# Kernel optimization log

Measured on AMD Instinct MI355X. Metric: run time of the kernel, lower is better.

## Reference

```python
import jax, jax.numpy as jnp
import numpy as np

N, E = 50000, 400000
FN, FE, FG = 32, 16, 16
H1, H2 = 256, 128


def seg_mean(x, idx, n):
    # mean of edge rows per segment; empty segments -> 0 (scatter_mean semantics)
    s = jax.ops.segment_sum(x, idx, num_segments=n)
    c = jax.ops.segment_sum(jnp.ones((x.shape[0], 1), x.dtype), idx, num_segments=n)
    return s / jnp.maximum(c, 1.0)


def setup_inputs() -> dict:
    key = jax.random.key(0)
    ks = jax.random.split(key, 32)
    g = lambda k, shape, s=0.05: jax.random.normal(k, shape, dtype=jnp.float32) * s
    return {
        'nodes': g(ks[0], (N, FN), 1.0),
        'edges': g(ks[1], (E, FE), 1.0),
        'globals_u': g(ks[2], (FG,), 1.0),
        'senders': jax.random.randint(ks[3], (E,), 0, N, dtype=jnp.int32),
        'receivers': jax.random.randint(ks[4], (E,), 0, N, dtype=jnp.int32),
        'We1': g(ks[5], (FE, H1)), 'be1': jnp.zeros((H1,), jnp.float32),
        'Wn1': g(ks[6], (FN, H1)), 'Win1': g(ks[7], (H1, H1)), 'Wout1': g(ks[8], (H1, H1)), 'bn1': jnp.zeros((H1,), jnp.float32),
        'Wu1': g(ks[9], (FG, H1)), 'Wgn1': g(ks[10], (H1, H1)), 'Wge1': g(ks[11], (H1, H1)), 'bu1': jnp.zeros((H1,), jnp.float32),
        'We2': g(ks[12], (H1, H2)), 'be2': jnp.zeros((H2,), jnp.float32),
        'Wn2': g(ks[13], (H1, H2)), 'Win2': g(ks[14], (H2, H2)), 'Wout2': g(ks[15], (H2, H2)), 'bn2': jnp.zeros((H2,), jnp.float32),
        'Wu2': g(ks[16], (H1, H2)), 'Wgn2': g(ks[17], (H2, H2)), 'Wge2': g(ks[18], (H2, H2)), 'bu2': jnp.zeros((H2,), jnp.float32),
    }


def reference(nodes, edges, globals_u, senders, receivers,
              We1, be1, Wn1, Win1, Wout1, bn1, Wu1, Wgn1, Wge1, bu1,
              We2, be2, Wn2, Win2, Wout2, bn2, Wu2, Wgn2, Wge2, bu2):
    n = nodes.shape[0]
    # --- block 1 (width 256) ---
    e1 = jax.nn.relu(edges @ We1 + be1)                                  # [E, H1]
    inc1 = seg_mean(e1, receivers, n)                                    # avg incoming edges per node
    out1 = seg_mean(e1, senders, n)                                      # avg outgoing edges per node
    n1 = jax.nn.relu(nodes @ Wn1 + inc1 @ Win1 + out1 @ Wout1 + bn1)     # [N, H1]
    u1 = jax.nn.relu(globals_u @ Wu1 + n1.mean(0) @ Wgn1 + e1.mean(0) @ Wge1 + bu1)  # [H1]
    # --- block 2 (width 128) ---
    e2 = jax.nn.relu(e1 @ We2 + be2)                                     # [E, H2]
    inc2 = seg_mean(e2, receivers, n)
    out2 = seg_mean(e2, senders, n)
    n2 = jax.nn.relu(n1 @ Wn2 + inc2 @ Win2 + out2 @ Wout2 + bn2)        # [N, H2]
    u2 = jax.nn.relu(u1 @ Wu2 + n2.mean(0) @ Wgn2 + e2.mean(0) @ Wge2 + bu2)  # [H2]
    return n2, e2, u2
```

## Files before the change

kernel.cpp:

```cpp
#include <hip/hip_runtime.h>
#include <hip/hip_bf16.h>
#include <stdint.h>

#define NN 50000
#define NE 400000
#define FN 32
#define FE 16
#define FG 16
#define H1 256
#define H2 128
#define M2 (2*NN)
#define SCAN_B 391
#define NPART 256

typedef unsigned short u16;
typedef __bf16 bfv8 __attribute__((ext_vector_type(8)));
typedef float f32v4 __attribute__((ext_vector_type(4)));
typedef u16 usv2 __attribute__((ext_vector_type(2)));
typedef u16 usv4 __attribute__((ext_vector_type(4)));
typedef u16 usv8 __attribute__((ext_vector_type(8)));

#define APK 264
#define AP2 136
#define EP1 40


__device__ __forceinline__ u16 f2b(float x){
  __hip_bfloat16 h = __float2bfloat16(x);
  return *reinterpret_cast<u16*>(&h);
}
__device__ __forceinline__ float bf2f(u16 u){
  union{uint32_t i; float f;} v; v.i = ((uint32_t)u) << 16; return v.f;
}

template<int NCK, int NNT, int PITCH>
__device__ __forceinline__ void gemm_tiles(const u16* a_s, const u16* __restrict__ pB,
                                           int w, int l, f32v4* acc)
{
  const int lr = l & 15, q = l >> 4;
  const bfv8* bp = (const bfv8*)pB;
  for (int ck = 0; ck < NCK; ck++){
    bfv8 a = *(const bfv8*)&a_s[(w*16 + lr)*PITCH + ck*32 + q*8];
    #pragma unroll
    for (int nt = 0; nt < NNT; nt++){
      bfv8 b = bp[(ck*NNT + nt)*64 + l];
      acc[nt] = __builtin_amdgcn_mfma_f32_16x16x32_bf16(a, b, acc[nt], 0, 0, 0);
    }
  }
}

template<int C4PR_LOG2>
__device__ __forceinline__ void stage_rows(u16* a_s, const float* __restrict__ src,
                                           long n0, int t)
{
  const int c4pr = 1 << C4PR_LOG2;
  for (int idx = t; idx < 64*c4pr; idx += 256){
    int row = idx >> C4PR_LOG2, c4 = idx & (c4pr - 1);
    long n = n0 + row;
    float x0=0.f, x1=0.f, x2=0.f, x3=0.f;
    if (n < NN){
      const float4 v = *(const float4*)&src[(n << (C4PR_LOG2 + 2)) + c4*4];
      x0 = v.x; x1 = v.y; x2 = v.z; x3 = v.w;
    }
    usv4 o; o.x = f2b(x0); o.y = f2b(x1); o.z = f2b(x2); o.w = f2b(x3);
    *(usv4*)&a_s[row*APK + c4*4] = o;
  }
}

struct PD { const float* src; u16* dst; int K, N, Ks, perm; };
struct PackArgs { PD d[8]; };

__global__ __launch_bounds__(64) void pack_weights(PackArgs A){
  int b = blockIdx.x, l = threadIdx.x;
  int mi = 0, base = 0;
  for (; mi < 8; mi++){
    int tiles = (A.d[mi].K >> 5) * (A.d[mi].N >> 4);
    if (b < base + tiles) break;
    base += tiles;
  }
  const PD d = A.d[mi];
  const int tile = b - base;
  const int ntn = d.N >> 4;
  const int ck = tile / ntn, nt = tile % ntn;
  const int lr = l & 15, q = l >> 4;
  const int col = nt*16 + lr;
  usv8 o;
  #pragma unroll
  for (int j = 0; j < 8; j++){
    int k = ck*32 + q*8 + j;
    int sk = (d.perm == 1) ? (((k & 15) << 4) | (k >> 4))
           : (d.perm == 2) ? (((k & 7) << 4) | (k >> 3))
           : k;
    o[j] = (k < d.Ks) ? f2b(d.src[(long)sk * d.N + col]) : (u16)0;
  }
  *(usv8*)&d.dst[((long)tile*64 + l)*8] = o;
}

__global__ __launch_bounds__(256) void csr_count(const int* __restrict__ recv,
    const int* __restrict__ send, int* cnt, int* pos_in, int* pos_out)
{
  int e = blockIdx.x*256 + threadIdx.x;
  if (e >= NE) return;
  pos_in [e] = atomicAdd(&cnt[recv[e]], 1);
  pos_out[e] = atomicAdd(&cnt[NN + send[e]], 1);
}

__global__ __launch_bounds__(256) void scan_blocks(const int* __restrict__ cnt,
    int* off, int* btot)
{
  __shared__ int s[256];
  int b = blockIdx.x, t = threadIdx.x;
  int i = b*256 + t;
  int v = (i < M2) ? cnt[i] : 0;
  s[t] = v; __syncthreads();
  int acc = v;
  for (int d = 1; d < 256; d <<= 1){
    int add = (t >= d) ? s[t-d] : 0;
    __syncthreads();
    acc += add; s[t] = acc;
    __syncthreads();
  }
  if (i < M2) off[i] = acc - v;
  if (t == 255) btot[b] = acc;
}

__global__ __launch_bounds__(256) void scan_tops(int* btot){
  __shared__ int s[512], ts[256];
  int t = threadIdx.x;
  s[t]     = (t < SCAN_B) ? btot[t] : 0;
  s[256+t] = (256+t < SCAN_B) ? btot[256+t] : 0;
  __syncthreads();
  int a0 = s[2*t], a1 = s[2*t+1];
  int tot = a0 + a1;
  ts[t] = tot; __syncthreads();
  int acc = tot;
  for (int d = 1; d < 256; d <<= 1){
    int add = (t >= d) ? ts[t-d] : 0;
    __syncthreads();
    acc += add; ts[t] = acc;
    __syncthreads();
  }
  int excl = acc - tot;
  if (2*t   < SCAN_B) btot[2*t]   = excl;
  if (2*t+1 < SCAN_B) btot[2*t+1] = excl + a0;
}

__global__ __launch_bounds__(256) void scan_fix(int* off, const int* __restrict__ btot){
  int i = blockIdx.x*256 + threadIdx.x;
  if (i < M2) off[i] += btot[blockIdx.x];
}

__global__ __launch_bounds__(256) void csr_fill(const int* __restrict__ recv,
    const int* __restrict__ send, const int* __restrict__ off,
    const int* __restrict__ pos_in, const int* __restrict__ pos_out, int* lis)
{
  int e = blockIdx.x*256 + threadIdx.x;
  if (e >= NE) return;
  lis[off[recv[e]]      + pos_in [e]] = e;
  lis[off[NN + send[e]] + pos_out[e]] = e;
}

__global__ __launch_bounds__(256) void edge1_kernel(const float* __restrict__ edges,
    const u16* __restrict__ pWe1, const float* __restrict__ be1,
    u16* __restrict__ e1b, float* __restrict__ e1p)
{
  __shared__ __align__(16) u16 a_es[64*EP1];
  __shared__ float cs_s[H1];
  __shared__ float bs[H1];
  const int t = threadIdx.x;
  const long e0 = (long)blockIdx.x * 64;
  const int w = t >> 6, l = t & 63, lr = l & 15, q = l >> 4;
  cs_s[t] = 0.f;
  bs[t] = be1[t];
  {
    int row = t >> 2, c4 = t & 3;
    float4 v = *(const float4*)&edges[(e0 + row)*FE + c4*4];
    usv4 o = { f2b(v.x), f2b(v.y), f2b(v.z), f2b(v.w) };
    *(usv4*)&a_es[row*EP1 + c4*4] = o;
    *(usv4*)&a_es[row*EP1 + 16 + c4*4] = (usv4){0,0,0,0};
  }
  __syncthreads();
  f32v4 acc[16];
  #pragma unroll
  for (int nt = 0; nt < 16; nt++) acc[nt] = (f32v4){0.f,0.f,0.f,0.f};
  gemm_tiles<1,16,EP1>(a_es, pWe1, w, l, acc);

  #pragma unroll
  for (int nt = 0; nt < 16; nt++){
    const float b = bs[nt*16 + lr];
    float part = 0.f;
    #pragma unroll
    for (int r = 0; r < 4; r++){
      float v = fmaxf(acc[nt][r] + b, 0.f);
      acc[nt][r] = v; part += v;
    }
    part += __shfl_xor(part, 16);
    part += __shfl_xor(part, 32);
    if (q == 0) atomicAdd(&cs_s[nt*16 + lr], part);
  }
  usv8 ob0[4], ob1[4];
  #pragma unroll
  for (int r = 0; r < 4; r++){
    #pragma unroll
    for (int h = 0; h < 8; h++){ ob0[r][h] = f2b(acc[h][r]); ob1[r][h] = f2b(acc[8+h][r]); }
  }
  __syncthreads();
  atomicAdd(&e1p[(blockIdx.x & (NPART-1))*H1 + t], cs_s[t]);
  #pragma unroll
  for (int r = 0; r < 4; r++){
    const int m = w*16 + q*4 + r;
    *(usv8*)&e1b[(e0 + m)*H1 + lr*16]     = ob0[r];
    *(usv8*)&e1b[(e0 + m)*H1 + lr*16 + 8] = ob1[r];
  }
}

template<bool WRB>
__global__ __launch_bounds__(256) void e2_kernel(float* __restrict__ e2f,
    const u16* __restrict__ pWe2, const float* __restrict__ be2, float* __restrict__ e2p,
    u16* __restrict__ e2b)
{
  __shared__ __align__(16) u16 a_s[64*APK];
  __shared__ float cs_s[H2];
  __shared__ float bs[H2];
  const int t = threadIdx.x;
  const long e0 = (long)blockIdx.x * 64;
  const int w = t >> 6, l = t & 63, lr = l & 15, q = l >> 4;
  if (t < H2){ cs_s[t] = 0.f; bs[t] = be2[t]; }
  const u16* e1u = (const u16*)e2f;
  for (int idx = t; idx < 64*32; idx += 256){
    int row = idx >> 5, ch = idx & 31;
    usv8 v = *(const usv8*)&e1u[(e0 + row)*H1 + ch*8];
    *(usv8*)&a_s[row*APK + ch*8] = v;
  }
  __syncthreads();
  f32v4 acc[8];
  #pragma unroll
  for (int nt = 0; nt < 8; nt++) acc[nt] = (f32v4){0.f,0.f,0.f,0.f};
  gemm_tiles<8,8,APK>(a_s, pWe2, w, l, acc);

  #pragma unroll
  for (int nt = 0; nt < 8; nt++){
    const float b = bs[nt*16 + lr];
    float part = 0.f;
    #pragma unroll
    for (int r = 0; r < 4; r++){
      float v = fmaxf(acc[nt][r] + b, 0.f);
      acc[nt][r] = v; part += v;
    }
    part += __shfl_xor(part, 16);
    part += __shfl_xor(part, 32);
    if (q == 0) atomicAdd(&cs_s[nt*16 + lr], part);
  }
  __syncthreads();
  float* fl = (float*)a_s;
  #pragma unroll
  for (int r = 0; r < 4; r++){
    const int m = w*16 + q*4 + r;
    const int sw = (m & 7) * 4;
    #pragma unroll
    for (int nt = 0; nt < 8; nt++)
      fl[m*128 + ((nt*16 + lr) ^ sw)] = acc[nt][r];
  }
  __syncthreads();
  if (t < H2) atomicAdd(&e2p[(blockIdx.x & (NPART-1))*H2 + t], cs_s[t]);
  {
    const int row = t >> 2, c = t & 3;
    const int sw = (row & 7) * 4;
    #pragma unroll
    for (int k = 0; k < 8; k++){
      const int wi = (c*32 + k*4) ^ sw;
      float4 v = *(const float4*)&fl[row*128 + wi];
      *(float4*)&e2f[(e0 + row)*H2 + c*32 + k*4] = v;
    }
  }
  if (WRB){
    #pragma unroll
    for (int r = 0; r < 4; r++){
      const int m = w*16 + q*4 + r;
      usv8 ob;
      #pragma unroll
      for (int nt = 0; nt < 8; nt++) ob[nt] = f2b(acc[nt][r]);
      *(usv8*)&e2b[(e0 + m)*H2 + lr*8] = ob;
    }
  }
}

template<int PITCH>
__device__ __forceinline__ void gather_h1(u16* a_s, const u16* __restrict__ src,
    const int* roff, const int* __restrict__ lis, int w, int l)
{
  for (int rr = 0; rr < 16; rr++){
    int r = w + rr*4;
    int rs = roff[r], re = roff[r+1];
    float s0=0.f, s1=0.f, s2=0.f, s3=0.f;
    int j = rs;
    for (; j + 8 <= re; j += 8){
      int i0=lis[j],i1=lis[j+1],i2=lis[j+2],i3=lis[j+3];
      int i4=lis[j+4],i5=lis[j+5],i6=lis[j+6],i7=lis[j+7];
      usv4 a0 = *(const usv4*)&src[(long)i0*H1 + l*4];
      usv4 a1 = *(const usv4*)&src[(long)i1*H1 + l*4];
      usv4 a2 = *(const usv4*)&src[(long)i2*H1 + l*4];
      usv4 a3 = *(const usv4*)&src[(long)i3*H1 + l*4];
      usv4 a4 = *(const usv4*)&src[(long)i4*H1 + l*4];
      usv4 a5 = *(const usv4*)&src[(long)i5*H1 + l*4];
      usv4 a6 = *(const usv4*)&src[(long)i6*H1 + l*4];
      usv4 a7 = *(const usv4*)&src[(long)i7*H1 + l*4];
      s0 += ((bf2f(a0.x)+bf2f(a1.x)) + (bf2f(a2.x)+bf2f(a3.x)))
          + ((bf2f(a4.x)+bf2f(a5.x)) + (bf2f(a6.x)+bf2f(a7.x)));
      s1 += ((bf2f(a0.y)+bf2f(a1.y)) + (bf2f(a2.y)+bf2f(a3.y)))
          + ((bf2f(a4.y)+bf2f(a5.y)) + (bf2f(a6.y)+bf2f(a7.y)));
      s2 += ((bf2f(a0.z)+bf2f(a1.z)) + (bf2f(a2.z)+bf2f(a3.z)))
          + ((bf2f(a4.z)+bf2f(a5.z)) + (bf2f(a6.z)+bf2f(a7.z)));
      s3 += ((bf2f(a0.w)+bf2f(a1.w)) + (bf2f(a2.w)+bf2f(a3.w)))
          + ((bf2f(a4.w)+bf2f(a5.w)) + (bf2f(a6.w)+bf2f(a7.w)));
    }
    for (; j + 4 <= re; j += 4){
      int i0=lis[j],i1=lis[j+1],i2=lis[j+2],i3=lis[j+3];
      usv4 a0 = *(const usv4*)&src[(long)i0*H1 + l*4];
      usv4 a1 = *(const usv4*)&src[(long)i1*H1 + l*4];
      usv4 a2 = *(const usv4*)&src[(long)i2*H1 + l*4];
      usv4 a3 = *(const usv4*)&src[(long)i3*H1 + l*4];
      s0 += (bf2f(a0.x)+bf2f(a1.x)) + (bf2f(a2.x)+bf2f(a3.x));
      s1 += (bf2f(a0.y)+bf2f(a1.y)) + (bf2f(a2.y)+bf2f(a3.y));
      s2 += (bf2f(a0.z)+bf2f(a1.z)) + (bf2f(a2.z)+bf2f(a3.z));
      s3 += (bf2f(a0.w)+bf2f(a1.w)) + (bf2f(a2.w)+bf2f(a3.w));
    }
    for (; j < re; ++j){
      int i0 = lis[j];
      usv4 a0 = *(const usv4*)&src[(long)i0*H1 + l*4];
      s0 += bf2f(a0.x); s1 += bf2f(a0.y); s2 += bf2f(a0.z); s3 += bf2f(a0.w);
    }
    float rd = 1.f / fmaxf((float)(re - rs), 1.f);
    usv4 o = { f2b(s0*rd), f2b(s1*rd), f2b(s2*rd), f2b(s3*rd) };
    *(usv4*)&a_s[r*PITCH + l*4] = o;
  }
}

template<int PITCH>
__device__ __forceinline__ void gather_h2(u16* a_s, const float* __restrict__ src,
    const int* roff, const int* __restrict__ lis, int w, int l)
{
  for (int rr = 0; rr < 16; rr++){
    int r = w + rr*4;
    int rs = roff[r], re = roff[r+1];
    float s0=0.f, s1=0.f;
    int j = rs;
    for (; j + 8 <= re; j += 8){
      int i0=lis[j],i1=lis[j+1],i2=lis[j+2],i3=lis[j+3];
      int i4=lis[j+4],i5=lis[j+5],i6=lis[j+6],i7=lis[j+7];
      float2 a0 = *(const float2*)&src[(long)i0*H2 + l*2];
      float2 a1 = *(const float2*)&src[(long)i1*H2 + l*2];
      float2 a2 = *(const float2*)&src[(long)i2*H2 + l*2];
      float2 a3 = *(const float2*)&src[(long)i3*H2 + l*2];
      float2 a4 = *(const float2*)&src[(long)i4*H2 + l*2];
      float2 a5 = *(const float2*)&src[(long)i5*H2 + l*2];
      float2 a6 = *(const float2*)&src[(long)i6*H2 + l*2];
      float2 a7 = *(const float2*)&src[(long)i7*H2 + l*2];
      s0 += ((a0.x+a1.x) + (a2.x+a3.x)) + ((a4.x+a5.x) + (a6.x+a7.x));
      s1 += ((a0.y+a1.y) + (a2.y+a3.y)) + ((a4.y+a5.y) + (a6.y+a7.y));
    }
    for (; j + 4 <= re; j += 4){
      int i0=lis[j],i1=lis[j+1],i2=lis[j+2],i3=lis[j+3];
      float2 a0 = *(const float2*)&src[(long)i0*H2 + l*2];
      float2 a1 = *(const float2*)&src[(long)i1*H2 + l*2];
      float2 a2 = *(const float2*)&src[(long)i2*H2 + l*2];
      float2 a3 = *(const float2*)&src[(long)i3*H2 + l*2];
      s0 += (a0.x+a1.x) + (a2.x+a3.x);
      s1 += (a0.y+a1.y) + (a2.y+a3.y);
    }
    for (; j < re; ++j){
      int i0 = lis[j];
      float2 a0 = *(const float2*)&src[(long)i0*H2 + l*2];
      s0 += a0.x; s1 += a0.y;
    }
    float rd = 1.f / fmaxf((float)(re - rs), 1.f);
    usv2 o = { f2b(s0*rd), f2b(s1*rd) };
    *(usv2*)&a_s[r*PITCH + l*2] = o;
  }
}

template<int PITCH>
__device__ __forceinline__ void gather_h2b(u16* a_s, const u16* __restrict__ src,
    const int* roff, const int* __restrict__ lis, int w, int l)
{
  for (int rr = 0; rr < 16; rr++){
    int r = w + rr*4;
    int rs = roff[r], re = roff[r+1];
    float s0=0.f, s1=0.f;
    int j = rs;
    for (; j + 8 <= re; j += 8){
      int i0=lis[j],i1=lis[j+1],i2=lis[j+2],i3=lis[j+3];
      int i4=lis[j+4],i5=lis[j+5],i6=lis[j+6],i7=lis[j+7];
      usv2 a0 = *(const usv2*)&src[(long)i0*H2 + l*2];
      usv2 a1 = *(const usv2*)&src[(long)i1*H2 + l*2];
      usv2 a2 = *(const usv2*)&src[(long)i2*H2 + l*2];
      usv2 a3 = *(const usv2*)&src[(long)i3*H2 + l*2];
      usv2 a4 = *(const usv2*)&src[(long)i4*H2 + l*2];
      usv2 a5 = *(const usv2*)&src[(long)i5*H2 + l*2];
      usv2 a6 = *(const usv2*)&src[(long)i6*H2 + l*2];
      usv2 a7 = *(const usv2*)&src[(long)i7*H2 + l*2];
      s0 += ((bf2f(a0.x)+bf2f(a1.x)) + (bf2f(a2.x)+bf2f(a3.x)))
          + ((bf2f(a4.x)+bf2f(a5.x)) + (bf2f(a6.x)+bf2f(a7.x)));
      s1 += ((bf2f(a0.y)+bf2f(a1.y)) + (bf2f(a2.y)+bf2f(a3.y)))
          + ((bf2f(a4.y)+bf2f(a5.y)) + (bf2f(a6.y)+bf2f(a7.y)));
    }
    for (; j + 4 <= re; j += 4){
      int i0=lis[j],i1=lis[j+1],i2=lis[j+2],i3=lis[j+3];
      usv2 a0 = *(const usv2*)&src[(long)i0*H2 + l*2];
      usv2 a1 = *(const usv2*)&src[(long)i1*H2 + l*2];
      usv2 a2 = *(const usv2*)&src[(long)i2*H2 + l*2];
      usv2 a3 = *(const usv2*)&src[(long)i3*H2 + l*2];
      s0 += (bf2f(a0.x)+bf2f(a1.x)) + (bf2f(a2.x)+bf2f(a3.x));
      s1 += (bf2f(a0.y)+bf2f(a1.y)) + (bf2f(a2.y)+bf2f(a3.y));
    }
    for (; j < re; ++j){
      int i0 = lis[j];
      usv2 a0 = *(const usv2*)&src[(long)i0*H2 + l*2];
      s0 += bf2f(a0.x); s1 += bf2f(a0.y);
    }
    float rd = 1.f / fmaxf((float)(re - rs), 1.f);
    usv2 o = { f2b(s0*rd), f2b(s1*rd) };
    *(usv2*)&a_s[r*PITCH + l*2] = o;
  }
}

__global__ __launch_bounds__(256, 4) void node1_kernel(
    const float* __restrict__ nodes, const u16* __restrict__ e1b,
    const int* __restrict__ off, const int* __restrict__ lis,
    const u16* __restrict__ pWn1, const u16* __restrict__ pWin1, const u16* __restrict__ pWout1,
    const float* __restrict__ bn1, u16* __restrict__ n1b, float* __restrict__ n1p)
{
  __shared__ __align__(16) u16 a_s[64*APK];
  __shared__ int roff[65], roff2[65];
  __shared__ float cs_s[H1];
  __shared__ float bs[H1];
  const int t = threadIdx.x;
  const long n0 = (long)blockIdx.x * 64;
  const int w = t >> 6, l = t & 63, lr = l & 15, q = l >> 4;

  cs_s[t] = 0.f;
  bs[t] = bn1[t];
  if (t <= 64){
    long idx = n0 + t;
    roff [t] = (idx >= NN) ? NE     : off[idx];
    roff2[t] = (idx >= NN) ? 2*NE   : off[NN + idx];
  }
  __syncthreads();

  f32v4 acc[16];
  #pragma unroll
  for (int nt = 0; nt < 16; nt++) acc[nt] = (f32v4){0.f,0.f,0.f,0.f};

  gather_h1<APK>(a_s, e1b, roff, lis, w, l);
  __syncthreads();
  gemm_tiles<8,16,APK>(a_s, pWin1, w, l, acc);
  __syncthreads();

  gather_h1<APK>(a_s, e1b, roff2, lis, w, l);
  __syncthreads();
  gemm_tiles<8,16,APK>(a_s, pWout1, w, l, acc);
  __syncthreads();

  stage_rows<3>(a_s, nodes, n0, t);
  __syncthreads();
  gemm_tiles<1,16,APK>(a_s, pWn1, w, l, acc);

  #pragma unroll
  for (int nt = 0; nt < 16; nt++){
    const float b = bs[nt*16 + lr];
    float part = 0.f;
    #pragma unroll
    for (int r = 0; r < 4; r++){
      const long n = n0 + w*16 + q*4 + r;
      float v = fmaxf(acc[nt][r] + b, 0.f);
      acc[nt][r] = v;
      if (n < NN) part += v;
    }
    part += __shfl_xor(part, 16);
    part += __shfl_xor(part, 32);
    if (q == 0) atomicAdd(&cs_s[nt*16 + lr], part);
  }
  __syncthreads();
  atomicAdd(&n1p[(blockIdx.x & (NPART-1))*H1 + t], cs_s[t]);
  #pragma unroll
  for (int r = 0; r < 4; r++){
    const int m = w*16 + q*4 + r;
    const long n = n0 + m;
    if (n < NN){
      usv8 o0, o1;
      #pragma unroll
      for (int h = 0; h < 8; h++){ o0[h] = f2b(acc[h][r]); o1[h] = f2b(acc[8+h][r]); }
      *(usv8*)&n1b[n*H1 + lr*16]     = o0;
      *(usv8*)&n1b[n*H1 + lr*16 + 8] = o1;
    }
  }
}

template<bool GB>
__global__ __launch_bounds__(256, 4) void node2_kernel(
    const u16* __restrict__ n1b, const float* __restrict__ e2f, const u16* __restrict__ e2b,
    const int* __restrict__ off, const int* __restrict__ lis,
    const u16* __restrict__ pWn2, const u16* __restrict__ pWin2, const u16* __restrict__ pWout2,
    const float* __restrict__ bn2, float* __restrict__ n2_out, float* __restrict__ n2p)
{
  __shared__ __align__(16) u16 a_s[64*AP2];
  __shared__ int roff[65], roff2[65];
  __shared__ float cs_s[H2];
  const int t = threadIdx.x;
  const long n0 = (long)blockIdx.x * 64;
  const int w = t >> 6, l = t & 63, lr = l & 15, q = l >> 4;

  if (t < H2) cs_s[t] = 0.f;
  if (t <= 64){
    long idx = n0 + t;
    roff [t] = (idx >= NN) ? NE     : off[idx];
    roff2[t] = (idx >= NN) ? 2*NE   : off[NN + idx];
  }
  __syncthreads();

  f32v4 acc[8];
  #pragma unroll
  for (int nt = 0; nt < 8; nt++) acc[nt] = (f32v4){0.f,0.f,0.f,0.f};

  for (int h = 0; h < 2; h++){
    for (int idx = t; idx < 64*16; idx += 256){
      int row = idx >> 4, ch = idx & 15;
      long n = n0 + row;
      usv8 v = (usv8){0,0,0,0,0,0,0,0};
      if (n < NN) v = *(const usv8*)&n1b[n*H1 + h*128 + ch*8];
      *(usv8*)&a_s[row*AP2 + ch*8] = v;
    }
    __syncthreads();
    gemm_tiles<4,8,AP2>(a_s, pWn2 + h*(4*8*64*8), w, l, acc);
    __syncthreads();
  }

  if (GB) gather_h2b<AP2>(a_s, e2b, roff, lis, w, l);
  else    gather_h2 <AP2>(a_s, e2f, roff, lis, w, l);
  __syncthreads();
  gemm_tiles<4,8,AP2>(a_s, pWin2, w, l, acc);
  __syncthreads();

  if (GB) gather_h2b<AP2>(a_s, e2b, roff2, lis, w, l);
  else    gather_h2 <AP2>(a_s, e2f, roff2, lis, w, l);
  __syncthreads();
  gemm_tiles<4,8,AP2>(a_s, pWout2, w, l, acc);

  #pragma unroll
  for (int nt = 0; nt < 8; nt++){
    const float b = bn2[nt*16 + lr];
    float part = 0.f;
    #pragma unroll
    for (int r = 0; r < 4; r++){
      const long n = n0 + w*16 + q*4 + r;
      float v = fmaxf(acc[nt][r] + b, 0.f);
      acc[nt][r] = v;
      if (n < NN) part += v;
    }
    part += __shfl_xor(part, 16);
    part += __shfl_xor(part, 32);
    if (q == 0) atomicAdd(&cs_s[nt*16 + lr], part);
  }
  __syncthreads();
  if (t < H2) atomicAdd(&n2p[(blockIdx.x & (NPART-1))*H2 + t], cs_s[t]);
  #pragma unroll
  for (int nt = 0; nt < 8; nt++){
    const int j = nt*16 + lr;
    #pragma unroll
    for (int r = 0; r < 4; r++){
      const long n = n0 + w*16 + q*4 + r;
      if (n < NN) n2_out[n*H2 + j] = acc[nt][r];
    }
  }
}

__global__ void u1_kernel(const float* __restrict__ gu, const float* __restrict__ Wu1,
    const float* __restrict__ Wgn1, const float* __restrict__ Wge1, const float* __restrict__ bu1,
    const float* __restrict__ n1p, const float* __restrict__ e1p, float* __restrict__ u1v)
{
    __shared__ float ncs[H1], ecs[H1];
    const int j = threadIdx.x;
    float sn = 0.f, se = 0.f;
    #pragma unroll 8
    for (int c = 0; c < NPART; c++){ sn += n1p[c*H1 + j]; se += e1p[c*H1 + j]; }
    ncs[j] = sn; ecs[j] = se;
    __syncthreads();
    float acc = bu1[j];
    #pragma unroll
    for (int k = 0; k < FG; k++) acc += gu[k] * Wu1[k*H1 + j];
    for (int k = 0; k < H1; k++) acc += (ncs[k] * (1.f/NN)) * Wgn1[k*H1 + j];
    for (int k = 0; k < H1; k++) acc += (ecs[k] * (1.f/NE)) * Wge1[k*H1 + j];
    u1v[j] = fmaxf(acc, 0.f);
}

__global__ void u2_kernel(const float* __restrict__ u1v, const float* __restrict__ Wu2,
    const float* __restrict__ Wgn2, const float* __restrict__ Wge2, const float* __restrict__ bu2,
    const float* __restrict__ n2p, const float* __restrict__ e2p, float* __restrict__ u2_out)
{
    __shared__ float ncs[H2], ecs[H2];
    const int j = threadIdx.x;
    float sn = 0.f, se = 0.f;
    #pragma unroll 8
    for (int c = 0; c < NPART; c++){ sn += n2p[c*H2 + j]; se += e2p[c*H2 + j]; }
    ncs[j] = sn; ecs[j] = se;
    __syncthreads();
    float acc = bu2[j];
    for (int k = 0; k < H1; k++) acc += u1v[k] * Wu2[k*H2 + j];
    for (int k = 0; k < H2; k++) acc += (ncs[k] * (1.f/NN)) * Wgn2[k*H2 + j];
    for (int k = 0; k < H2; k++) acc += (ecs[k] * (1.f/NE)) * Wge2[k*H2 + j];
    u2_out[j] = fmaxf(acc, 0.f);
}

extern "C" void kernel_launch(void* const* d_in, const int* in_sizes, int n_in,
                              void* d_out, int out_size, void* d_ws, size_t ws_size,
                              hipStream_t stream)
{
    (void)in_sizes; (void)n_in; (void)out_size;
    const float* nodes = (const float*)d_in[0];
    const float* edges = (const float*)d_in[1];
    const float* gu    = (const float*)d_in[2];
    const int* senders   = (const int*)d_in[3];
    const int* receivers = (const int*)d_in[4];
    const float* We1  = (const float*)d_in[5];  const float* be1 = (const float*)d_in[6];
    const float* Wn1  = (const float*)d_in[7];  const float* Win1= (const float*)d_in[8];
    const float* Wout1= (const float*)d_in[9];  const float* bn1 = (const float*)d_in[10];
    const float* Wu1  = (const float*)d_in[11]; const float* Wgn1= (const float*)d_in[12];
    const float* Wge1 = (const float*)d_in[13]; const float* bu1 = (const float*)d_in[14];
    const float* We2  = (const float*)d_in[15]; const float* be2 = (const float*)d_in[16];
    const float* Wn2  = (const float*)d_in[17]; const float* Win2= (const float*)d_in[18];
    const float* Wout2= (const float*)d_in[19]; const float* bn2 = (const float*)d_in[20];
    const float* Wu2  = (const float*)d_in[21]; const float* Wgn2= (const float*)d_in[22];
    const float* Wge2 = (const float*)d_in[23]; const float* bu2 = (const float*)d_in[24];

    float* ws = (float*)d_ws;
    size_t o = 0;
    int*   cnt    = (int*)(ws + o);  o += M2;
    float* e1p    = ws + o;          o += (size_t)NPART*H1;
    float* n1p    = ws + o;          o += (size_t)NPART*H1;
    float* e2p    = ws + o;          o += (size_t)NPART*H2;
    float* n2p    = ws + o;          o += (size_t)NPART*H2;
    const size_t zero_bytes = o * sizeof(float);
    float* u1v    = ws + o;          o += 256;
    int*   off    = (int*)(ws + o);  o += M2;
    int*   pos_in = (int*)(ws + o);  o += NE;
    int*   pos_out= (int*)(ws + o);  o += NE;
    int*   lis    = (int*)(ws + o);  o += 2*NE;
    int*   btot   = (int*)(ws + o);  o += 400;

    u16* pbase = (u16*)(ws + o);
    size_t po = 0;
    u16* pWin1 = pbase + po;  po += (size_t)H1*H1;
    u16* pWout1= pbase + po;  po += (size_t)H1*H1;
    u16* pWn1  = pbase + po;  po += (size_t)FN*H1;
    u16* pWe1  = pbase + po;  po += (size_t)32*H1;
    u16* pWe2  = pbase + po;  po += (size_t)H1*H2;
    u16* pWn2  = pbase + po;  po += (size_t)H1*H2;
    u16* pWin2 = pbase + po;  po += (size_t)H2*H2;
    u16* pWout2= pbase + po;  po += (size_t)H2*H2;
    o += (po + 1) / 2;

    u16* n1b = (u16*)(ws + o);
    o += (size_t)NN*H1/2;
    u16* e2b = (u16*)(ws + o);
    const bool useb = ws_size >= (o + (size_t)NE*H2/2) * sizeof(float);

    float* n2_out = (float*)d_out;
    float* e2f    = n2_out + (size_t)NN*H2;
    float* u2_out = n2_out + (size_t)(NN + NE)*H2;
    u16*   e1b    = (u16*)e2f;

    hipMemsetAsync(d_ws, 0, zero_bytes, stream);

    PackArgs pa;
    pa.d[0] = {Win1,  pWin1,  H1, H1, H1, 1};
    pa.d[1] = {Wout1, pWout1, H1, H1, H1, 1};
    pa.d[2] = {Wn1,   pWn1,   FN, H1, FN, 0};
    pa.d[3] = {We1,   pWe1,   32, H1, FE, 0};
    pa.d[4] = {We2,   pWe2,   H1, H2, H1, 1};
    pa.d[5] = {Wn2,   pWn2,   H1, H2, H1, 1};
    pa.d[6] = {Win2,  pWin2,  H2, H2, H2, useb ? 2 : 0};
    pa.d[7] = {Wout2, pWout2, H2, H2, H2, useb ? 2 : 0};
    int total_tiles = 0;
    for (int i = 0; i < 8; i++) total_tiles += (pa.d[i].K >> 5) * (pa.d[i].N >> 4);
    pack_weights<<<total_tiles, 64, 0, stream>>>(pa);

    const int EG = (NE + 255)/256;
    csr_count<<<EG, 256, 0, stream>>>(receivers, senders, cnt, pos_in, pos_out);
    scan_blocks<<<SCAN_B, 256, 0, stream>>>(cnt, off, btot);
    scan_tops<<<1, 256, 0, stream>>>(btot);
    scan_fix<<<SCAN_B, 256, 0, stream>>>(off, btot);
    csr_fill<<<EG, 256, 0, stream>>>(receivers, senders, off, pos_in, pos_out, lis);

    edge1_kernel<<<NE/64, 256, 0, stream>>>(edges, pWe1, be1, e1b, e1p);

    node1_kernel<<<(NN + 63)/64, 256, 0, stream>>>(nodes, e1b, off, lis,
        pWn1, pWin1, pWout1, bn1, n1b, n1p);

    u1_kernel<<<1, H1, 0, stream>>>(gu, Wu1, Wgn1, Wge1, bu1, n1p, e1p, u1v);

    if (useb){
      e2_kernel<true ><<<NE/64, 256, 0, stream>>>(e2f, pWe2, be2, e2p, e2b);
      node2_kernel<true ><<<(NN + 63)/64, 256, 0, stream>>>(n1b, e2f, e2b, off, lis,
          pWn2, pWin2, pWout2, bn2, n2_out, n2p);
    } else {
      e2_kernel<false><<<NE/64, 256, 0, stream>>>(e2f, pWe2, be2, e2p, e2b);
      node2_kernel<false><<<(NN + 63)/64, 256, 0, stream>>>(n1b, e2f, e2b, off, lis,
          pWn2, pWin2, pWout2, bn2, n2_out, n2p);
    }

    u2_kernel<<<1, H2, 0, stream>>>(u1v, Wu2, Wgn2, Wge2, bu2, n2p, e2p, u2_out);
}
```

Baseline: 907.4 us.

## Scatter edge features into CSR-sorted copies so node kernels stream contiguously

csr_fill now records each edge's CSR slot for both receiver and sender lists, plus a sibling map from receiver slot to sender slot. Edge kernels write their bf16 outputs twice, once into a receiver-sorted copy and once into a sender-sorted copy. The node kernels can then sum each segment by reading contiguous rows instead of following index lists. The edge-2 kernel processes edges in receiver-CSR order and scatters its fp32 output back to the original positions. This replaces random gathers with streaming reads, at the cost of scattered writes, twice as much edge storage and a larger workspace. The 8-wide unrolled gather loops are also removed.

```diff
diff --git a/kernel.cpp b/kernel.cpp
--- a/kernel.cpp
+++ b/kernel.cpp
@@ -152,26 +152,35 @@
 
 __global__ __launch_bounds__(256) void csr_fill(const int* __restrict__ recv,
     const int* __restrict__ send, const int* __restrict__ off,
-    const int* __restrict__ pos_in, const int* __restrict__ pos_out, int* lis)
+    int* pos_in, int* pos_out, int* lis, int* sib)
 {
   int e = blockIdx.x*256 + threadIdx.x;
   if (e >= NE) return;
-  lis[off[recv[e]]      + pos_in [e]] = e;
-  lis[off[NN + send[e]] + pos_out[e]] = e;
-}
-
+  int pi = off[recv[e]]      + pos_in [e];
+  int po = off[NN + send[e]] + pos_out[e];
+  lis[pi] = e;
+  lis[po] = e;
+  pos_in [e] = pi;
+  pos_out[e] = po;
+  sib[pi] = po;
+}
+
+template<bool S1>
 __global__ __launch_bounds__(256) void edge1_kernel(const float* __restrict__ edges,
     const u16* __restrict__ pWe1, const float* __restrict__ be1,
-    u16* __restrict__ e1b, float* __restrict__ e1p)
+    u16* __restrict__ e1b, float* __restrict__ e1p,
+    u16* __restrict__ es1, const int* __restrict__ pin, const int* __restrict__ pout)
 {
   __shared__ __align__(16) u16 a_es[64*EP1];
   __shared__ float cs_s[H1];
   __shared__ float bs[H1];
+  __shared__ int pin_s[64], pout_s[64];
   const int t = threadIdx.x;
   const long e0 = (long)blockIdx.x * 64;
   const int w = t >> 6, l = t & 63, lr = l & 15, q = l >> 4;
   cs_s[t] = 0.f;
   bs[t] = be1[t];
+  if (S1 && t < 64){ pin_s[t] = pin[e0 + t]; pout_s[t] = pout[e0 + t]; }
   {
     int row = t >> 2, c4 = t & 3;
     float4 v = *(const float4*)&edges[(e0 + row)*FE + c4*4];
@@ -209,28 +218,51 @@
   #pragma unroll
   for (int r = 0; r < 4; r++){
     const int m = w*16 + q*4 + r;
-    *(usv8*)&e1b[(e0 + m)*H1 + lr*16]     = ob0[r];
-    *(usv8*)&e1b[(e0 + m)*H1 + lr*16 + 8] = ob1[r];
-  }
-}
-
-template<bool WRB>
+    if (S1){
+      const long pr = pin_s[m], ps = pout_s[m];
+      *(usv8*)&es1[pr*H1 + lr*16]     = ob0[r];
+      *(usv8*)&es1[pr*H1 + lr*16 + 8] = ob1[r];
+      *(usv8*)&es1[ps*H1 + lr*16]     = ob0[r];
+      *(usv8*)&es1[ps*H1 + lr*16 + 8] = ob1[r];
+    } else {
+      *(usv8*)&e1b[(e0 + m)*H1 + lr*16]     = ob0[r];
+      *(usv8*)&e1b[(e0 + m)*H1 + lr*16 + 8] = ob1[r];
+    }
+  }
+}
+
+template<bool S1, bool S2>
 __global__ __launch_bounds__(256) void e2_kernel(float* __restrict__ e2f,
     const u16* __restrict__ pWe2, const float* __restrict__ be2, float* __restrict__ e2p,
-    u16* __restrict__ e2b)
+    u16* __restrict__ es2, const u16* __restrict__ es1,
+    const int* __restrict__ lis, const int* __restrict__ sib,
+    const int* __restrict__ pin, const int* __restrict__ pout)
 {
   __shared__ __align__(16) u16 a_s[64*APK];
   __shared__ float cs_s[H2];
   __shared__ float bs[H2];
+  __shared__ int ta[64], tb[64];
   const int t = threadIdx.x;
   const long e0 = (long)blockIdx.x * 64;
   const int w = t >> 6, l = t & 63, lr = l & 15, q = l >> 4;
   if (t < H2){ cs_s[t] = 0.f; bs[t] = be2[t]; }
-  const u16* e1u = (const u16*)e2f;
-  for (int idx = t; idx < 64*32; idx += 256){
-    int row = idx >> 5, ch = idx & 31;
-    usv8 v = *(const usv8*)&e1u[(e0 + row)*H1 + ch*8];
-    *(usv8*)&a_s[row*APK + ch*8] = v;
+  if (t < 64){
+    if (S1){ ta[t] = lis[e0 + t]; tb[t] = sib[e0 + t]; }
+    else if (S2){ ta[t] = pin[e0 + t]; tb[t] = pout[e0 + t]; }
+  }
+  if (S1){
+    for (int idx = t; idx < 64*32; idx += 256){
+      int row = idx >> 5, ch = idx & 31;
+      usv8 v = *(const usv8*)&es1[(e0 + row)*H1 + ch*8];
+      *(usv8*)&a_s[row*APK + ch*8] = v;
+    }
+  } else {
+    const u16* e1u = (const u16*)e2f;
+    for (int idx = t; idx < 64*32; idx += 256){
+      int row = idx >> 5, ch = idx & 31;
+      usv8 v = *(const usv8*)&e1u[(e0 + row)*H1 + ch*8];
+      *(usv8*)&a_s[row*APK + ch*8] = v;
+    }
   }
   __syncthreads();
   f32v4 acc[8];
@@ -265,22 +297,26 @@
   if (t < H2) atomicAdd(&e2p[(blockIdx.x & (NPART-1))*H2 + t], cs_s[t]);
   {
     const int row = t >> 2, c = t & 3;
+    const long orow = S1 ? (long)ta[row] : (e0 + row);
     const int sw = (row & 7) * 4;
     #pragma unroll
     for (int k = 0; k < 8; k++){
       const int wi = (c*32 + k*4) ^ sw;
       float4 v = *(const float4*)&fl[row*128 + wi];
-      *(float4*)&e2f[(e0 + row)*H2 + c*32 + k*4] = v;
-    }
-  }
-  if (WRB){
+      *(float4*)&e2f[orow*H2 + c*32 + k*4] = v;
+    }
+  }
+  if (S2){
     #pragma unroll
     for (int r = 0; r < 4; r++){
       const int m = w*16 + q*4 + r;
       usv8 ob;
       #pragma unroll
       for (int nt = 0; nt < 8; nt++) ob[nt] = f2b(acc[nt][r]);
-      *(usv8*)&e2b[(e0 + m)*H2 + lr*8] = ob;
+      const long pr = S1 ? (e0 + m) : (long)ta[m];
+      const long ps = tb[m];
+      *(usv8*)&es2[pr*H2 + lr*8] = ob;
+      *(usv8*)&es2[ps*H2 + lr*8] = ob;
     }
   }
 }
@@ -294,26 +330,6 @@
     int rs = roff[r], re = roff[r+1];
     float s0=0.f, s1=0.f, s2=0.f, s3=0.f;
     int j = rs;
-    for (; j + 8 <= re; j += 8){
-      int i0=lis[j],i1=lis[j+1],i2=lis[j+2],i3=lis[j+3];
-      int i4=lis[j+4],i5=lis[j+5],i6=lis[j+6],i7=lis[j+7];
-      usv4 a0 = *(const usv4*)&src[(long)i0*H1 + l*4];
-      usv4 a1 = *(const usv4*)&src[(long)i1*H1 + l*4];
-      usv4 a2 = *(const usv4*)&src[(long)i2*H1 + l*4];
-      usv4 a3 = *(const usv4*)&src[(long)i3*H1 + l*4];
-      usv4 a4 = *(const usv4*)&src[(long)i4*H1 + l*4];
-      usv4 a5 = *(const usv4*)&src[(long)i5*H1 + l*4];
-      usv4 a6 = *(const usv4*)&src[(long)i6*H1 + l*4];
-      usv4 a7 = *(const usv4*)&src[(long)i7*H1 + l*4];
-      s0 += ((bf2f(a0.x)+bf2f(a1.x)) + (bf2f(a2.x)+bf2f(a3.x)))
-          + ((bf2f(a4.x)+bf2f(a5.x)) + (bf2f(a6.x)+bf2f(a7.x)));
-      s1 += ((bf2f(a0.y)+bf2f(a1.y)) + (bf2f(a2.y)+bf2f(a3.y)))
-          + ((bf2f(a4.y)+bf2f(a5.y)) + (bf2f(a6.y)+bf2f(a7.y)));
-      s2 += ((bf2f(a0.z)+bf2f(a1.z)) + (bf2f(a2.z)+bf2f(a3.z)))
-          + ((bf2f(a4.z)+bf2f(a5.z)) + (bf2f(a6.z)+bf2f(a7.z)));
-      s3 += ((bf2f(a0.w)+bf2f(a1.w)) + (bf2f(a2.w)+bf2f(a3.w)))
-          + ((bf2f(a4.w)+bf2f(a5.w)) + (bf2f(a6.w)+bf2f(a7.w)));
-    }
     for (; j + 4 <= re; j += 4){
       int i0=lis[j],i1=lis[j+1],i2=lis[j+2],i3=lis[j+3];
       usv4 a0 = *(const usv4*)&src[(long)i0*H1 + l*4];
@@ -345,20 +361,6 @@
     int rs = roff[r], re = roff[r+1];
     float s0=0.f, s1=0.f;
     int j = rs;
-    for (; j + 8 <= re; j += 8){
-      int i0=lis[j],i1=lis[j+1],i2=lis[j+2],i3=lis[j+3];
-      int i4=lis[j+4],i5=lis[j+5],i6=lis[j+6],i7=lis[j+7];
-      float2 a0 = *(const float2*)&src[(long)i0*H2 + l*2];
-      float2 a1 = *(const float2*)&src[(long)i1*H2 + l*2];
-      float2 a2 = *(const float2*)&src[(long)i2*H2 + l*2];
-      float2 a3 = *(const float2*)&src[(long)i3*H2 + l*2];
-      float2 a4 = *(const float2*)&src[(long)i4*H2 + l*2];
-      float2 a5 = *(const float2*)&src[(long)i5*H2 + l*2];
-      float2 a6 = *(const float2*)&src[(long)i6*H2 + l*2];
-      float2 a7 = *(const float2*)&src[(long)i7*H2 + l*2];
-      s0 += ((a0.x+a1.x) + (a2.x+a3.x)) + ((a4.x+a5.x) + (a6.x+a7.x));
-      s1 += ((a0.y+a1.y) + (a2.y+a3.y)) + ((a4.y+a5.y) + (a6.y+a7.y));
-    }
     for (; j + 4 <= re; j += 4){
       int i0=lis[j],i1=lis[j+1],i2=lis[j+2],i3=lis[j+3];
       float2 a0 = *(const float2*)&src[(long)i0*H2 + l*2];
@@ -380,42 +382,53 @@
 }
 
 template<int PITCH>
-__device__ __forceinline__ void gather_h2b(u16* a_s, const u16* __restrict__ src,
-    const int* roff, const int* __restrict__ lis, int w, int l)
+__device__ __forceinline__ void stream_h1(u16* a_s, const u16* __restrict__ src,
+    const int* roff, int w, int l)
+{
+  for (int rr = 0; rr < 16; rr++){
+    int r = w + rr*4;
+    int rs = roff[r], re = roff[r+1];
+    float s0=0.f, s1=0.f, s2=0.f, s3=0.f;
+    int j = rs;
+    for (; j + 4 <= re; j += 4){
+      usv4 a0 = *(const usv4*)&src[(long)(j  )*H1 + l*4];
+      usv4 a1 = *(const usv4*)&src[(long)(j+1)*H1 + l*4];
+      usv4 a2 = *(const usv4*)&src[(long)(j+2)*H1 + l*4];
+      usv4 a3 = *(const usv4*)&src[(long)(j+3)*H1 + l*4];
+      s0 += (bf2f(a0.x)+bf2f(a1.x)) + (bf2f(a2.x)+bf2f(a3.x));
+      s1 += (bf2f(a0.y)+bf2f(a1.y)) + (bf2f(a2.y)+bf2f(a3.y));
+      s2 += (bf2f(a0.z)+bf2f(a1.z)) + (bf2f(a2.z)+bf2f(a3.z));
+      s3 += (bf2f(a0.w)+bf2f(a1.w)) + (bf2f(a2.w)+bf2f(a3.w));
+    }
+    for (; j < re; ++j){
+      usv4 a0 = *(const usv4*)&src[(long)j*H1 + l*4];
+      s0 += bf2f(a0.x); s1 += bf2f(a0.y); s2 += bf2f(a0.z); s3 += bf2f(a0.w);
+    }
+    float rd = 1.f / fmaxf((float)(re - rs), 1.f);
+    usv4 o = { f2b(s0*rd), f2b(s1*rd), f2b(s2*rd), f2b(s3*rd) };
+    *(usv4*)&a_s[r*PITCH + l*4] = o;
+  }
+}
+
+template<int PITCH>
+__device__ __forceinline__ void stream_h2(u16* a_s, const u16* __restrict__ src,
+    const int* roff, int w, int l)
 {
   for (int rr = 0; rr < 16; rr++){
     int r = w + rr*4;
     int rs = roff[r], re = roff[r+1];
     float s0=0.f, s1=0.f;
     int j = rs;
-    for (; j + 8 <= re; j += 8){
-      int i0=lis[j],i1=lis[j+1],i2=lis[j+2],i3=lis[j+3];
-      int i4=lis[j+4],i5=lis[j+5],i6=lis[j+6],i7=lis[j+7];
-      usv2 a0 = *(const usv2*)&src[(long)i0*H2 + l*2];
-      usv2 a1 = *(const usv2*)&src[(long)i1*H2 + l*2];
-      usv2 a2 = *(const usv2*)&src[(long)i2*H2 + l*2];
-      usv2 a3 = *(const usv2*)&src[(long)i3*H2 + l*2];
-      usv2 a4 = *(const usv2*)&src[(long)i4*H2 + l*2];
-      usv2 a5 = *(const usv2*)&src[(long)i5*H2 + l*2];
-      usv2 a6 = *(const usv2*)&src[(long)i6*H2 + l*2];
-      usv2 a7 = *(const usv2*)&src[(long)i7*H2 + l*2];
-      s0 += ((bf2f(a0.x)+bf2f(a1.x)) + (bf2f(a2.x)+bf2f(a3.x)))
-          + ((bf2f(a4.x)+bf2f(a5.x)) + (bf2f(a6.x)+bf2f(a7.x)));
-      s1 += ((bf2f(a0.y)+bf2f(a1.y)) + (bf2f(a2.y)+bf2f(a3.y)))
-          + ((bf2f(a4.y)+bf2f(a5.y)) + (bf2f(a6.y)+bf2f(a7.y)));
-    }
     for (; j + 4 <= re; j += 4){
-      int i0=lis[j],i1=lis[j+1],i2=lis[j+2],i3=lis[j+3];
-      usv2 a0 = *(const usv2*)&src[(long)i0*H2 + l*2];
-      usv2 a1 = *(const usv2*)&src[(long)i1*H2 + l*2];
-      usv2 a2 = *(const usv2*)&src[(long)i2*H2 + l*2];
-      usv2 a3 = *(const usv2*)&src[(long)i3*H2 + l*2];
+      usv2 a0 = *(const usv2*)&src[(long)(j  )*H2 + l*2];
+      usv2 a1 = *(const usv2*)&src[(long)(j+1)*H2 + l*2];
+      usv2 a2 = *(const usv2*)&src[(long)(j+2)*H2 + l*2];
+      usv2 a3 = *(const usv2*)&src[(long)(j+3)*H2 + l*2];
       s0 += (bf2f(a0.x)+bf2f(a1.x)) + (bf2f(a2.x)+bf2f(a3.x));
       s1 += (bf2f(a0.y)+bf2f(a1.y)) + (bf2f(a2.y)+bf2f(a3.y));
     }
     for (; j < re; ++j){
-      int i0 = lis[j];
-      usv2 a0 = *(const usv2*)&src[(long)i0*H2 + l*2];
+      usv2 a0 = *(const usv2*)&src[(long)j*H2 + l*2];
       s0 += bf2f(a0.x); s1 += bf2f(a0.y);
     }
     float rd = 1.f / fmaxf((float)(re - rs), 1.f);
@@ -424,8 +437,9 @@
   }
 }
 
+template<bool S1>
 __global__ __launch_bounds__(256, 4) void node1_kernel(
-    const float* __restrict__ nodes, const u16* __restrict__ e1b,
+    const float* __restrict__ nodes, const u16* __restrict__ e1b, const u16* __restrict__ es1,
     const int* __restrict__ off, const int* __restrict__ lis,
     const u16* __restrict__ pWn1, const u16* __restrict__ pWin1, const u16* __restrict__ pWout1,
     const float* __restrict__ bn1, u16* __restrict__ n1b, float* __restrict__ n1p)
@@ -451,12 +465,14 @@
   #pragma unroll
   for (int nt = 0; nt < 16; nt++) acc[nt] = (f32v4){0.f,0.f,0.f,0.f};
 
-  gather_h1<APK>(a_s, e1b, roff, lis, w, l);
+  if (S1) stream_h1<APK>(a_s, es1, roff, w, l);
+  else    gather_h1<APK>(a_s, e1b, roff, lis, w, l);
   __syncthreads();
   gemm_tiles<8,16,APK>(a_s, pWin1, w, l, acc);
   __syncthreads();
 
-  gather_h1<APK>(a_s, e1b, roff2, lis, w, l);
+  if (S1) stream_h1<APK>(a_s, es1, roff2, w, l);
+  else    gather_h1<APK>(a_s, e1b, roff2, lis, w, l);
   __syncthreads();
   gemm_tiles<8,16,APK>(a_s, pWout1, w, l, acc);
   __syncthreads();
@@ -496,9 +512,9 @@
   }
 }
 
-template<bool GB>
+template<bool S2>
 __global__ __launch_bounds__(256, 4) void node2_kernel(
-    const u16* __restrict__ n1b, const float* __restrict__ e2f, const u16* __restrict__ e2b,
+    const u16* __restrict__ n1b, const float* __restrict__ e2f, const u16* __restrict__ es2,
     const int* __restrict__ off, const int* __restrict__ lis,
     const u16* __restrict__ pWn2, const u16* __restrict__ pWin2, const u16* __restrict__ pWout2,
     const float* __restrict__ bn2, float* __restrict__ n2_out, float* __restrict__ n2p)
@@ -535,14 +551,14 @@
     __syncthreads();
   }
 
-  if (GB) gather_h2b<AP2>(a_s, e2b, roff, lis, w, l);
-  else    gather_h2 <AP2>(a_s, e2f, roff, lis, w, l);
+  if (S2) stream_h2<AP2>(a_s, es2, roff, w, l);
+  else    gather_h2<AP2>(a_s, e2f, roff, lis, w, l);
   __syncthreads();
   gemm_tiles<4,8,AP2>(a_s, pWin2, w, l, acc);
   __syncthreads();
 
-  if (GB) gather_h2b<AP2>(a_s, e2b, roff2, lis, w, l);
-  else    gather_h2 <AP2>(a_s, e2f, roff2, lis, w, l);
+  if (S2) stream_h2<AP2>(a_s, es2, roff2, w, l);
+  else    gather_h2<AP2>(a_s, e2f, roff2, lis, w, l);
   __syncthreads();
   gemm_tiles<4,8,AP2>(a_s, pWout2, w, l, acc);
 
@@ -642,9 +658,10 @@
     const size_t zero_bytes = o * sizeof(float);
     float* u1v    = ws + o;          o += 256;
     int*   off    = (int*)(ws + o);  o += M2;
-    int*   pos_in = (int*)(ws + o);  o += NE;
-    int*   pos_out= (int*)(ws + o);  o += NE;
+    int*   pin    = (int*)(ws + o);  o += NE;
+    int*   pout   = (int*)(ws + o);  o += NE;
     int*   lis    = (int*)(ws + o);  o += 2*NE;
+    int*   sib    = (int*)(ws + o);  o += NE;
     int*   btot   = (int*)(ws + o);  o += 400;
 
     u16* pbase = (u16*)(ws + o);
@@ -661,8 +678,11 @@
 
     u16* n1b = (u16*)(ws + o);
     o += (size_t)NN*H1/2;
-    u16* e2b = (u16*)(ws + o);
-    const bool useb = ws_size >= (o + (size_t)NE*H2/2) * sizeof(float);
+    u16* es2 = (u16*)(ws + o);
+    const bool S2 = ws_size >= (o + (size_t)2*NE*H2/2) * sizeof(float);
+    if (S2) o += (size_t)2*NE*H2/2;
+    u16* es1 = (u16*)(ws + o);
+    const bool S1 = S2 && ws_size >= (o + (size_t)2*NE*H1/2) * sizeof(float);
 
     float* n2_out = (float*)d_out;
     float* e2f    = n2_out + (size_t)NN*H2;
@@ -678,33 +698,43 @@
     pa.d[3] = {We1,   pWe1,   32, H1, FE, 0};
     pa.d[4] = {We2,   pWe2,   H1, H2, H1, 1};
     pa.d[5] = {Wn2,   pWn2,   H1, H2, H1, 1};
-    pa.d[6] = {Win2,  pWin2,  H2, H2, H2, useb ? 2 : 0};
-    pa.d[7] = {Wout2, pWout2, H2, H2, H2, useb ? 2 : 0};
+    pa.d[6] = {Win2,  pWin2,  H2, H2, H2, S2 ? 2 : 0};
+    pa.d[7] = {Wout2, pWout2, H2, H2, H2, S2 ? 2 : 0};
     int total_tiles = 0;
     for (int i = 0; i < 8; i++) total_tiles += (pa.d[i].K >> 5) * (pa.d[i].N >> 4);
     pack_weights<<<total_tiles, 64, 0, stream>>>(pa);
 
     const int EG = (NE + 255)/256;
-    csr_count<<<EG, 256, 0, stream>>>(receivers, senders, cnt, pos_in, pos_out);
+    csr_count<<<EG, 256, 0, stream>>>(receivers, senders, cnt, pin, pout);
     scan_blocks<<<SCAN_B, 256, 0, stream>>>(cnt, off, btot);
     scan_tops<<<1, 256, 0, stream>>>(btot);
     scan_fix<<<SCAN_B, 256, 0, stream>>>(off, btot);
-    csr_fill<<<EG, 256, 0, stream>>>(receivers, senders, off, pos_in, pos_out, lis);
-
-    edge1_kernel<<<NE/64, 256, 0, stream>>>(edges, pWe1, be1, e1b, e1p);
-
-    node1_kernel<<<(NN + 63)/64, 256, 0, stream>>>(nodes, e1b, off, lis,
-        pWn1, pWin1, pWout1, bn1, n1b, n1p);
-
-    u1_kernel<<<1, H1, 0, stream>>>(gu, Wu1, Wgn1, Wge1, bu1, n1p, e1p, u1v);
-
-    if (useb){
-      e2_kernel<true ><<<NE/64, 256, 0, stream>>>(e2f, pWe2, be2, e2p, e2b);
-      node2_kernel<true ><<<(NN + 63)/64, 256, 0, stream>>>(n1b, e2f, e2b, off, lis,
+    csr_fill<<<EG, 256, 0, stream>>>(receivers, senders, off, pin, pout, lis, sib);
+
+    const int NG = (NN + 63)/64;
+    if (S1){
+      edge1_kernel<true ><<<NE/64, 256, 0, stream>>>(edges, pWe1, be1, e1b, e1p, es1, pin, pout);
+      node1_kernel<true ><<<NG, 256, 0, stream>>>(nodes, e1b, es1, off, lis,
+          pWn1, pWin1, pWout1, bn1, n1b, n1p);
+      u1_kernel<<<1, H1, 0, stream>>>(gu, Wu1, Wgn1, Wge1, bu1, n1p, e1p, u1v);
+      e2_kernel<true,true><<<NE/64, 256, 0, stream>>>(e2f, pWe2, be2, e2p, es2, es1, lis, sib, pin, pout);
+      node2_kernel<true ><<<NG, 256, 0, stream>>>(n1b, e2f, es2, off, lis,
+          pWn2, pWin2, pWout2, bn2, n2_out, n2p);
+    } else if (S2){
+      edge1_kernel<false><<<NE/64, 256, 0, stream>>>(edges, pWe1, be1, e1b, e1p, es1, pin, pout);
+      node1_kernel<false><<<NG, 256, 0, stream>>>(nodes, e1b, es1, off, lis,
+          pWn1, pWin1, pWout1, bn1, n1b, n1p);
+      u1_kernel<<<1, H1, 0, stream>>>(gu, Wu1, Wgn1, Wge1, bu1, n1p, e1p, u1v);
+      e2_kernel<false,true><<<NE/64, 256, 0, stream>>>(e2f, pWe2, be2, e2p, es2, es1, lis, sib, pin, pout);
+      node2_kernel<true ><<<NG, 256, 0, stream>>>(n1b, e2f, es2, off, lis,
           pWn2, pWin2, pWout2, bn2, n2_out, n2p);
     } else {
-      e2_kernel<false><<<NE/64, 256, 0, stream>>>(e2f, pWe2, be2, e2p, e2b);
-      node2_kernel<false><<<(NN + 63)/64, 256, 0, stream>>>(n1b, e2f, e2b, off, lis,
+      edge1_kernel<false><<<NE/64, 256, 0, stream>>>(edges, pWe1, be1, e1b, e1p, es1, pin, pout);
+      node1_kernel<false><<<NG, 256, 0, stream>>>(nodes, e1b, es1, off, lis,
+          pWn1, pWin1, pWout1, bn1, n1b, n1p);
+      u1_kernel<<<1, H1, 0, stream>>>(gu, Wu1, Wgn1, Wge1, bu1, n1p, e1p, u1v);
+      e2_kernel<false,false><<<NE/64, 256, 0, stream>>>(e2f, pWe2, be2, e2p, es2, es1, lis, sib, pin, pout);
+      node2_kernel<false><<<NG, 256, 0, stream>>>(n1b, e2f, es2, off, lis,
           pWn2, pWin2, pWout2, bn2, n2_out, n2p);
     }
 
```

Measured after the change: 1.065 ms. 1.17x slower.
